# Optimization experiments

Hardware: AMD Instinct MI355X
Metric: run time of the kernel (lower is better)

Reference implementation:

```python
import jax, jax.numpy as jnp
import numpy as np

HIDDEN = 768
HEADS = 12
HEAD_DIM = 64
SEQ = 512
DS_K = 64  # downsampling_k
EPS = 1e-6


def setup_inputs() -> dict:
    key = jax.random.key(0)
    ks = jax.random.split(key, 16)
    B = 32
    sd = 1.0 / DS_K
    glorot = jax.nn.initializers.lecun_normal()  # flax default_kernel_init
    inp = {
        "query": jax.random.normal(ks[0], (B, SEQ, HIDDEN), jnp.float32),
        "key": jax.random.normal(ks[1], (B, SEQ, HIDDEN), jnp.float32),
        "value": jax.random.normal(ks[2], (B, SEQ, HIDDEN), jnp.float32),
        "step": 0,
        # learned Linformer-style downsampling projections [k, s]
        "W_kds": sd * jax.random.normal(ks[3], (DS_K, SEQ), jnp.float32),
        "W_vds": sd * jax.random.normal(ks[4], (DS_K, SEQ), jnp.float32),
        # DenseGeneral qkv kernels [d, n, h] and biases [n, h]
        "Wq": glorot(ks[5], (HIDDEN, HEADS, HEAD_DIM), jnp.float32),
        "bq": jnp.zeros((HEADS, HEAD_DIM), jnp.float32),
        "Wk": glorot(ks[6], (HIDDEN, HEADS, HEAD_DIM), jnp.float32),
        "bk": jnp.zeros((HEADS, HEAD_DIM), jnp.float32),
        "Wv": glorot(ks[7], (HIDDEN, HEADS, HEAD_DIM), jnp.float32),
        "bv": jnp.zeros((HEADS, HEAD_DIM), jnp.float32),
        # out projection contracts (n, h) -> hidden
        "Wout": glorot(ks[8], (HEADS * HEAD_DIM, HIDDEN), jnp.float32).reshape(HEADS, HEAD_DIM, HIDDEN),
        "bout": jnp.zeros((HIDDEN,), jnp.float32),
    }
    return inp


def reference(query, key, value, step, W_kds, W_vds, Wq, bq, Wk, bk, Wv, bv, Wout, bout):
    # Linformer-style downsample of keys/values along sequence: [b,s,d] -> [b,k,d]
    key_ds = jnp.einsum("ks,bsd->bkd", W_kds, key)
    val_ds = jnp.einsum("ks,bsd->bkd", W_vds, value)

    # per-head projections
    queries = jnp.einsum("bqd,dnh->bqnh", query, Wq) + bq    # [b,q,n,h]
    keys = jnp.einsum("bkd,dnh->bknh", key_ds, Wk) + bk      # [b,k,n,h]
    values = jnp.einsum("bkd,dnh->bknh", val_ds, Wv) + bv    # [b,k,n,h]

    # kernelized linear attention with elu feature map (mask=False path)
    phi_q = jax.nn.elu(queries) + 1.0
    phi_k = jax.nn.elu(keys) + 1.0
    s = jnp.einsum("bknd,bknh->bndh", phi_k, values)          # [b,n,h,h] KV state
    z = jnp.sum(phi_k, axis=1)                                 # [b,n,h]
    qs = jnp.einsum("bqnd,bndh->bqnh", phi_q, s)
    qz = jnp.einsum("bqnd,bnd->bqn", phi_q, z) + EPS
    a_v = qs / qz[..., None]                                   # [b,q,n,h]

    out = jnp.einsum("bqnh,nhD->bqD", a_v, Wout) + bout        # [b,q,hidden]
    return out
```

## Files before the change

kernel.cpp:

```cpp
#include <hip/hip_runtime.h>

typedef unsigned short u16;
typedef u16 u16x8 __attribute__((ext_vector_type(8)));
typedef __bf16 bf16;
typedef bf16 bf16x8 __attribute__((ext_vector_type(8)));
typedef float f32x4 __attribute__((ext_vector_type(4)));

__device__ __forceinline__ float bf2f(u16 v) {
  union { unsigned u; float f; } x; x.u = ((unsigned)v) << 16; return x.f;
}
__device__ __forceinline__ u16 f2bf(float f) {
  union { float f; unsigned u; } x; x.f = f;
  unsigned u = x.u;
  u += 0x7fffu + ((u >> 16) & 1u);
  return (u16)(u >> 16);
}

#define GLDS16(g, l) __builtin_amdgcn_global_load_lds( \
    (const __attribute__((address_space(1))) unsigned int*)(const void*)(g), \
    (__attribute__((address_space(3))) unsigned int*)(void*)(l), 16, 0, 0)

__global__ __launch_bounds__(256) void prep_k(
    const float* __restrict__ Wq, const float* __restrict__ Wk,
    const float* __restrict__ Wv, const float* __restrict__ Wout,
    const float* __restrict__ query,
    const float* __restrict__ wkds, const float* __restrict__ wvds,
    const float* __restrict__ b0, const float* __restrict__ b1,
    const float* __restrict__ b2, const float* __restrict__ b3,
    u16* __restrict__ WT, u16* __restrict__ q_bf,
    u16* __restrict__ dstW, u16* __restrict__ dstB)
{
  __shared__ u16 T[64][72];
  const int blk = blockIdx.x;
  const int t = threadIdx.x;
  if (blk < 576) {
    const int bz = blk / 144, rr = blk % 144;
    const int r0 = (rr / 12) * 64, c0 = (rr % 12) * 64;
    const float* W = (bz == 0) ? Wq : (bz == 1) ? Wk : (bz == 2) ? Wv : Wout;
    u16* O = WT + (size_t)bz * 768 * 768;
    #pragma unroll
    for (int p = 0; p < 2; ++p) {
      int v = t + p * 256;
      int r = v / 8, c = (v % 8) * 8;
      f32x4 x0 = *(const f32x4*)&W[(size_t)(r0 + r) * 768 + c0 + c];
      f32x4 x1 = *(const f32x4*)&W[(size_t)(r0 + r) * 768 + c0 + c + 4];
      #pragma unroll
      for (int i = 0; i < 4; ++i) { T[r][c + i] = f2bf(x0[i]); T[r][c + 4 + i] = f2bf(x1[i]); }
    }
    __syncthreads();
    #pragma unroll
    for (int p = 0; p < 2; ++p) {
      int v = t + p * 256;
      int r = v / 8, c = (v % 8) * 8;
      u16x8 tv;
      #pragma unroll
      for (int i = 0; i < 8; ++i) tv[i] = T[c + i][r];
      *(u16x8*)&O[(size_t)(c0 + r) * 768 + r0 + c] = tv;
    }
  } else if (blk < 6720) {
    const size_t i = (size_t)(blk - 576) * 256 + t;
    f32x4 a = *(const f32x4*)&query[i * 8];
    f32x4 b = *(const f32x4*)&query[i * 8 + 4];
    u16x8 w;
    #pragma unroll
    for (int j = 0; j < 4; ++j) { w[j] = f2bf(a[j]); w[4 + j] = f2bf(b[j]); }
    *(u16x8*)&q_bf[i * 8] = w;
  } else {
    const int i = (blk - 6720) * 256 + t;
    if (i < 32768)      dstW[i] = f2bf(wkds[i]);
    else if (i < 65536) dstW[i] = f2bf(wvds[i - 32768]);
    else {
      int j = i - 65536, s = j / 768, si = j % 768;
      const float* src = (s == 0) ? b0 : (s == 1) ? b1 : (s == 2) ? b2 : b3;
      dstB[j] = f2bf(src[si]);
    }
  }
}

__global__ __launch_bounds__(256) void ds_k(
    const u16* __restrict__ Wds,
    const float* __restrict__ key, const float* __restrict__ value,
    u16* __restrict__ key_ds)
{
  __shared__ u16 As[64][40];
  __shared__ u16 Bs[128][36];
  const int pair = blockIdx.y >> 5, b = blockIdx.y & 31;
  const float* src = (pair ? value : key) + (size_t)b * 512 * 768;
  const u16* W = Wds + pair * 32768;
  u16* dst = key_ds + (size_t)pair * 1572864 + (size_t)b * 49152;
  const int nt = blockIdx.x * 128;
  const int t = threadIdx.x, wave = t >> 6, lane = t & 63;
  const int wm = (wave >> 1) * 32, wn = (wave & 1) * 64;
  const int lrow = lane & 15, quad = lane >> 4;
  const int kk = t >> 5, n4 = (t & 31) * 4;

  f32x4 acc[2][4] = {};
  for (int k0 = 0; k0 < 512; k0 += 32) {
    __syncthreads();
    {
      int r = t >> 2, c = (t & 3) * 8;
      *(u16x8*)&As[r][c] = *(const u16x8*)&W[(size_t)r * 512 + k0 + c];
    }
    #pragma unroll
    for (int p = 0; p < 4; ++p) {
      int k = kk + p * 8;
      f32x4 x = *(const f32x4*)&src[(size_t)(k0 + k) * 768 + nt + n4];
      #pragma unroll
      for (int i = 0; i < 4; ++i) Bs[n4 + i][k] = f2bf(x[i]);
    }
    __syncthreads();
    bf16x8 av[2], bv[4];
    #pragma unroll
    for (int i = 0; i < 2; ++i) av[i] = *(const bf16x8*)&As[wm + i * 16 + lrow][quad * 8];
    #pragma unroll
    for (int j = 0; j < 4; ++j) bv[j] = *(const bf16x8*)&Bs[wn + j * 16 + lrow][quad * 8];
    #pragma unroll
    for (int i = 0; i < 2; ++i)
      #pragma unroll
      for (int j = 0; j < 4; ++j)
        acc[i][j] = __builtin_amdgcn_mfma_f32_16x16x32_bf16(av[i], bv[j], acc[i][j], 0, 0, 0);
  }
  #pragma unroll
  for (int i = 0; i < 2; ++i)
    #pragma unroll
    for (int j = 0; j < 4; ++j) {
      const int col = nt + wn + j * 16 + lrow;
      #pragma unroll
      for (int r = 0; r < 4; ++r) {
        const int row = wm + i * 16 + quad * 4 + r;
        dst[(size_t)row * 768 + col] = f2bf(acc[i][j][r]);
      }
    }
}

template<int ACT, bool OF32>
__global__ __launch_bounds__(256) void gemm97_k(
    const u16* __restrict__ A, int lda,
    const u16* __restrict__ Bt, int ldb,
    void* __restrict__ Craw, int ldc,
    const u16* __restrict__ bias, int K)
{
  __shared__ u16 As[128 * 32];
  __shared__ u16 Bs[128 * 32];
  const int mt = blockIdx.x * 128, nt = blockIdx.y * 128;
  const int t = threadIdx.x, wave = t >> 6, lane = t & 63;
  const int wm = (wave >> 1) * 64, wn = (wave & 1) * 64;
  const int lrow = lane & 15, quad = lane >> 4;
  f32x4 acc[4][4] = {};

  for (int k0 = 0; k0 < K; k0 += 32) {
    __syncthreads();
    #pragma unroll
    for (int p = 0; p < 2; ++p) {
      const int s = wave * 128 + p * 64 + lane;
      const int r = s >> 2, c = (s & 3) * 8;
      const int lb = (wave * 128 + p * 64) * 8;
      GLDS16(&A[(size_t)(mt + r) * lda + k0 + c], &As[lb]);
      GLDS16(&Bt[(size_t)(nt + r) * ldb + k0 + c], &Bs[lb]);
    }
    __syncthreads();

    bf16x8 av[4], bv[4];
    #pragma unroll
    for (int i = 0; i < 4; ++i) av[i] = *(const bf16x8*)&As[(wm + i * 16 + lrow) * 32 + quad * 8];
    #pragma unroll
    for (int j = 0; j < 4; ++j) bv[j] = *(const bf16x8*)&Bs[(wn + j * 16 + lrow) * 32 + quad * 8];
    #pragma unroll
    for (int i = 0; i < 4; ++i)
      #pragma unroll
      for (int j = 0; j < 4; ++j)
        acc[i][j] = __builtin_amdgcn_mfma_f32_16x16x32_bf16(av[i], bv[j], acc[i][j], 0, 0, 0);
  }

  #pragma unroll
  for (int i = 0; i < 4; ++i) {
    #pragma unroll
    for (int j = 0; j < 4; ++j) {
      const int col = nt + wn + j * 16 + lrow;
      const float badd = bias ? bf2f(bias[col]) : 0.0f;
      #pragma unroll
      for (int r = 0; r < 4; ++r) {
        const int row = mt + wm + i * 16 + quad * 4 + r;
        float v = acc[i][j][r] + badd;
        if constexpr (ACT == 1) v = v > 0.0f ? v + 1.0f : __expf(v);
        if constexpr (OF32) ((float*)Craw)[(size_t)row * ldc + col] = v;
        else                ((u16*)Craw)[(size_t)row * ldc + col] = f2bf(v);
      }
    }
  }
}

template<int BM, int BN, int BK, int WM, int WN>
__global__ __launch_bounds__(256) void gemmkv_k(
    const u16* __restrict__ A, int lda,
    const u16* __restrict__ B, int ldb,
    u16* __restrict__ C, int ldc,
    const u16* __restrict__ bias,
    int K,
    long long offA_b, long long offB_b, long long offC_b, long long offBias_b)
{
  constexpr int LDSK = BK + 8;
  __shared__ u16 As[BM][LDSK];
  __shared__ u16 Bs[BN][LDSK];
  const int bb = blockIdx.z;
  A += bb * offA_b; B += bb * offB_b; C += bb * offC_b; bias += bb * offBias_b;
  const int mt = blockIdx.x * BM;
  const int nt = blockIdx.y * BN;
  const int t = threadIdx.x;
  const int wave = t >> 6, lane = t & 63;
  constexpr int WAVES_N = BN / WN;
  const int wm = (wave / WAVES_N) * WM;
  const int wn = (wave % WAVES_N) * WN;
  constexpr int FM = WM / 16, FN = WN / 16;
  const int lrow = lane & 15, quad = lane >> 4;
  f32x4 acc[FM][FN] = {};

  for (int k0 = 0; k0 < K; k0 += BK) {
    __syncthreads();
    #pragma unroll
    for (int p = 0; p < (BM * BK / 8) / 256; ++p) {
      int v = t + p * 256;
      int r = v / (BK / 8), c = (v % (BK / 8)) * 8;
      *(u16x8*)&As[r][c] = *(const u16x8*)&A[(size_t)(mt + r) * lda + k0 + c];
    }
    #pragma unroll
    for (int p = 0; p < (BN * BK / 8) / 256; ++p) {
      int v = t + p * 256;
      int r = v / (BK / 8), c = (v % (BK / 8)) * 8;
      *(u16x8*)&Bs[r][c] = *(const u16x8*)&B[(size_t)(nt + r) * ldb + k0 + c];
    }
    __syncthreads();
    bf16x8 av[FM], bv[FN];
    #pragma unroll
    for (int i = 0; i < FM; ++i) av[i] = *(const bf16x8*)&As[wm + i * 16 + lrow][quad * 8];
    #pragma unroll
    for (int j = 0; j < FN; ++j) bv[j] = *(const bf16x8*)&Bs[wn + j * 16 + lrow][quad * 8];
    #pragma unroll
    for (int i = 0; i < FM; ++i)
      #pragma unroll
      for (int j = 0; j < FN; ++j)
        acc[i][j] = __builtin_amdgcn_mfma_f32_16x16x32_bf16(av[i], bv[j], acc[i][j], 0, 0, 0);
  }
  #pragma unroll
  for (int i = 0; i < FM; ++i)
    #pragma unroll
    for (int j = 0; j < FN; ++j) {
      const int col = nt + wn + j * 16 + lrow;
      const float badd = bf2f(bias[col]);
      #pragma unroll
      for (int r = 0; r < 4; ++r) {
        const int row = mt + wm + i * 16 + quad * 4 + r;
        float v = acc[i][j][r] + badd;
        if (bb == 0) v = v > 0.0f ? v + 1.0f : __expf(v);
        C[(size_t)row * ldc + col] = f2bf(v);
      }
    }
}

__global__ __launch_bounds__(256) void kv_state_k(
    const u16* __restrict__ phi_k, const u16* __restrict__ vals,
    u16* __restrict__ sT, float* __restrict__ z)
{
  __shared__ float pk[64][65];
  __shared__ float vv[64][65];
  const int x = blockIdx.x;
  const int b = x / 12, n = x % 12;
  const int t = threadIdx.x;
  const u16* pkg = phi_k + (size_t)b * 64 * 768 + n * 64;
  const u16* vvg = vals  + (size_t)b * 64 * 768 + n * 64;
  #pragma unroll
  for (int p = 0; p < 2; ++p) {
    int v = t + p * 256;
    int r = v / 8, c = (v % 8) * 8;
    u16x8 a  = *(const u16x8*)&pkg[(size_t)r * 768 + c];
    u16x8 bq = *(const u16x8*)&vvg[(size_t)r * 768 + c];
    #pragma unroll
    for (int i = 0; i < 8; ++i) { pk[r][c + i] = bf2f(a[i]); vv[r][c + i] = bf2f(bq[i]); }
  }
  __syncthreads();
  const int d0 = (t >> 4) * 4, h0 = (t & 15) * 4;
  float s4[4][4] = {};
  for (int k = 0; k < 64; ++k) {
    float pv[4], vb[4];
    #pragma unroll
    for (int i = 0; i < 4; ++i) { pv[i] = pk[k][d0 + i]; vb[i] = vv[k][h0 + i]; }
    #pragma unroll
    for (int i = 0; i < 4; ++i)
      #pragma unroll
      for (int j = 0; j < 4; ++j) s4[i][j] += pv[i] * vb[j];
  }
  const size_t base = (size_t)x * 4096;
  #pragma unroll
  for (int i = 0; i < 4; ++i)
    #pragma unroll
    for (int j = 0; j < 4; ++j)
      sT[base + (size_t)(h0 + j) * 64 + d0 + i] = f2bf(s4[i][j]);
  if (t < 64) {
    float zz = 0.f;
    for (int k = 0; k < 64; ++k) zz += pk[k][t];
    z[(size_t)x * 64 + t] = zz;
  }
}

__global__ __launch_bounds__(256) void attn_av_k(
    u16* __restrict__ phi_q, const u16* __restrict__ sT, const float* __restrict__ zbuf)
{
  __shared__ u16 As[64 * 72];
  __shared__ u16 Bs[64 * 72];
  __shared__ float zv[64];
  __shared__ float zpart[4][64];
  __shared__ float zq[64];
  const int x = blockIdx.x, y = blockIdx.y;
  const int b = y / 12, n = y % 12;
  const int t = threadIdx.x;
  u16* Abase = phi_q + (size_t)b * 512 * 768 + (size_t)x * 64 * 768 + n * 64;
  const u16* Bbase = sT + (size_t)y * 4096;
  if (t < 64) zv[t] = zbuf[(size_t)y * 64 + t];
  #pragma unroll
  for (int p = 0; p < 2; ++p) {
    int v = t + p * 256;
    int r = v >> 3, c = (v & 7) * 8;
    *(u16x8*)&As[r * 72 + c] = *(const u16x8*)&Abase[(size_t)r * 768 + c];
    *(u16x8*)&Bs[r * 72 + c] = *(const u16x8*)&Bbase[r * 64 + c];
  }
  __syncthreads();
  {
    int r = t & 63, seg = t >> 6;
    float s = 0.f;
    #pragma unroll
    for (int j = 0; j < 16; ++j) s += bf2f(As[r * 72 + seg * 16 + j]) * zv[seg * 16 + j];
    zpart[seg][r] = s;
  }
  __syncthreads();
  if (t < 64) {
    float s = zpart[0][t] + zpart[1][t] + zpart[2][t] + zpart[3][t];
    zq[t] = 1.0f / (s + 1e-6f);
  }
  const int wave = t >> 6, lane = t & 63;
  const int wm = (wave >> 1) * 32, wn = (wave & 1) * 32;
  const int lrow = lane & 15, quad = lane >> 4;
  f32x4 acc[2][2] = {};
  #pragma unroll
  for (int c = 0; c < 2; ++c) {
    bf16x8 av[2], bv[2];
    #pragma unroll
    for (int i = 0; i < 2; ++i) av[i] = *(const bf16x8*)&As[(wm + i * 16 + lrow) * 72 + c * 32 + quad * 8];
    #pragma unroll
    for (int j = 0; j < 2; ++j) bv[j] = *(const bf16x8*)&Bs[(wn + j * 16 + lrow) * 72 + c * 32 + quad * 8];
    #pragma unroll
    for (int i = 0; i < 2; ++i)
      #pragma unroll
      for (int j = 0; j < 2; ++j)
        acc[i][j] = __builtin_amdgcn_mfma_f32_16x16x32_bf16(av[i], bv[j], acc[i][j], 0, 0, 0);
  }
  __syncthreads();
  #pragma unroll
  for (int i = 0; i < 2; ++i)
    #pragma unroll
    for (int j = 0; j < 2; ++j) {
      const int col = wn + j * 16 + lrow;
      #pragma unroll
      for (int r = 0; r < 4; ++r) {
        const int row = wm + i * 16 + quad * 4 + r;
        Abase[(size_t)row * 768 + col] = f2bf(acc[i][j][r] * zq[row]);
      }
    }
}

__global__ void tagfill_k(float* out, float val, int n) {
  int i = blockIdx.x * 256 + threadIdx.x;
  if (i < n) out[i] = val;
}

extern "C" void kernel_launch(void* const* d_in, const int* in_sizes, int n_in,
                              void* d_out, int out_size, void* d_ws, size_t ws_size,
                              hipStream_t stream) {
  (void)out_size;
  float* out = (float*)d_out;

  int o;
  if (n_in >= 14 && in_sizes[3] == 1) o = 4;
  else if (n_in == 13) o = 3;
  else { tagfill_k<<<4, 256, 0, stream>>>(out, 77.0f, 1024); return; }
  if (in_sizes[0] != 12582912 || in_sizes[o + 0] != 32768 || in_sizes[o + 2] != 589824) {
    tagfill_k<<<4, 256, 0, stream>>>(out, 88.0f, 1024); return;
  }

  const float* query = (const float*)d_in[0];
  const float* key   = (const float*)d_in[1];
  const float* value = (const float*)d_in[2];
  const float* W_kds = (const float*)d_in[o + 0];
  const float* W_vds = (const float*)d_in[o + 1];
  const float* Wq   = (const float*)d_in[o + 2];
  const float* bq   = (const float*)d_in[o + 3];
  const float* Wk   = (const float*)d_in[o + 4];
  const float* bk   = (const float*)d_in[o + 5];
  const float* Wv   = (const float*)d_in[o + 6];
  const float* bv   = (const float*)d_in[o + 7];
  const float* Wout = (const float*)d_in[o + 8];
  const float* bout = (const float*)d_in[o + 9];

  const size_t NEED = 55187456;
  if (ws_size < NEED) { tagfill_k<<<4, 256, 0, stream>>>(out, 123.0f, 1024); return; }

  char* base = (char*)d_ws;
  u16*   WT     = (u16*)base;
  char*  Breg   = base + 4718592;
  u16*   q_bf   = (u16*)Breg;
  u16*   key_ds = (u16*)Breg;
  u16*   sT     = (u16*)Breg;
  float* zbuf   = (float*)(Breg + 3145728);
  u16*   phi_k  = (u16*)(Breg + 6291456);
  u16*   vals   = (u16*)(Breg + 9437184);
  u16*   phi_q  = (u16*)(base + 29884416);
  u16*   Wds_c  = (u16*)(base + 55050240);
  u16*   bias_c = (u16*)(base + 55181312);
  u16* a_v = phi_q;
  u16* WqT   = WT;
  u16* WkT   = WT + 768 * 768;
  u16* WoutT = WT + 3 * 768 * 768;
  u16* bq_c = bias_c, *bk_c = bias_c + 768, *bout_c = bias_c + 2304;

  prep_k<<<6988, 256, 0, stream>>>(Wq, Wk, Wv, Wout, query, W_kds, W_vds,
                                   bq, bk, bv, bout, WT, q_bf, Wds_c, bias_c);

  gemm97_k<1, false><<<dim3(128, 6), 256, 0, stream>>>(
      q_bf, 768, WqT, 768, phi_q, 768, bq_c, 768);

  ds_k<<<dim3(6, 64), 256, 0, stream>>>(Wds_c, key, value, key_ds);

  gemmkv_k<64, 64, 32, 32, 32><<<dim3(32, 12, 2), 256, 0, stream>>>(
      key_ds, 768, WkT, 768, phi_k, 768, bk_c, 768,
      1572864, 589824, 1572864, 768);

  kv_state_k<<<dim3(384), 256, 0, stream>>>(phi_k, vals, sT, zbuf);

  attn_av_k<<<dim3(8, 384), 256, 0, stream>>>(phi_q, sT, zbuf);

  gemm97_k<0, true><<<dim3(128, 6), 256, 0, stream>>>(
      a_v, 768, WoutT, 768, out, 768, bout_c, 768);
}
```

Measured before the change: 312.6 us.

## Pipeline Linformer downsample kernel with register prefetch and double-buffered LDS

The downsample GEMM kernel is restructured. Its N tile shrinks from 128 to 64 columns, doubling the grid to 768 blocks. The A operand (W_ds) now goes straight from global memory into registers, and the fp32 key/value tile is prefetched into registers one K-step ahead. A double-buffered LDS tile allows one barrier per iteration instead of two. The aim is to hide global-load latency and raise occupancy on this memory-bound pass over the key and value tensors, at the cost of per-column scalar strided loads instead of float4 loads.

```diff
diff --git a/kernel.cpp b/kernel.cpp
--- a/kernel.cpp
+++ b/kernel.cpp
@@ -82,48 +82,59 @@
     const float* __restrict__ key, const float* __restrict__ value,
     u16* __restrict__ key_ds)
 {
-  __shared__ u16 As[64][40];
-  __shared__ u16 Bs[128][36];
+  __shared__ u16 Bs[2][64 * 40];
   const int pair = blockIdx.y >> 5, b = blockIdx.y & 31;
   const float* src = (pair ? value : key) + (size_t)b * 512 * 768;
   const u16* W = Wds + pair * 32768;
   u16* dst = key_ds + (size_t)pair * 1572864 + (size_t)b * 49152;
-  const int nt = blockIdx.x * 128;
+  const int nt = blockIdx.x * 64;
   const int t = threadIdx.x, wave = t >> 6, lane = t & 63;
-  const int wm = (wave >> 1) * 32, wn = (wave & 1) * 64;
+  const int wm = (wave >> 1) * 32, wn = (wave & 1) * 32;
   const int lrow = lane & 15, quad = lane >> 4;
-  const int kk = t >> 5, n4 = (t & 31) * 4;
-
-  f32x4 acc[2][4] = {};
-  for (int k0 = 0; k0 < 512; k0 += 32) {
-    __syncthreads();
-    {
-      int r = t >> 2, c = (t & 3) * 8;
-      *(u16x8*)&As[r][c] = *(const u16x8*)&W[(size_t)r * 512 + k0 + c];
-    }
-    #pragma unroll
-    for (int p = 0; p < 4; ++p) {
-      int k = kk + p * 8;
-      f32x4 x = *(const f32x4*)&src[(size_t)(k0 + k) * 768 + nt + n4];
-      #pragma unroll
-      for (int i = 0; i < 4; ++i) Bs[n4 + i][k] = f2bf(x[i]);
-    }
-    __syncthreads();
-    bf16x8 av[2], bv[4];
-    #pragma unroll
-    for (int i = 0; i < 2; ++i) av[i] = *(const bf16x8*)&As[wm + i * 16 + lrow][quad * 8];
-    #pragma unroll
-    for (int j = 0; j < 4; ++j) bv[j] = *(const bf16x8*)&Bs[wn + j * 16 + lrow][quad * 8];
+  const int bn = t & 63, bk8 = (t >> 6) * 8;
+  const float* bcol = src + nt + bn;
+
+  f32x4 acc[2][2] = {};
+  float breg[8];
+  bf16x8 av[2][2];
+
+  #pragma unroll
+  for (int i = 0; i < 8; ++i) breg[i] = bcol[(size_t)(bk8 + i) * 768];
+  #pragma unroll
+  for (int i = 0; i < 2; ++i)
+    av[0][i] = *(const bf16x8*)&W[(size_t)(wm + i * 16 + lrow) * 512 + quad * 8];
+
+  #pragma unroll
+  for (int step = 0; step < 16; ++step) {
+    const int cur = step & 1, nxt = cur ^ 1;
+    u16x8 wv;
+    #pragma unroll
+    for (int i = 0; i < 8; ++i) wv[i] = f2bf(breg[i]);
+    *(u16x8*)&Bs[cur][bn * 40 + bk8] = wv;
+    if (step < 15) {
+      const int k1 = (step + 1) * 32;
+      #pragma unroll
+      for (int i = 0; i < 8; ++i) breg[i] = bcol[(size_t)(k1 + bk8 + i) * 768];
+      #pragma unroll
+      for (int i = 0; i < 2; ++i)
+        av[nxt][i] = *(const bf16x8*)&W[(size_t)(wm + i * 16 + lrow) * 512 + k1 + quad * 8];
+    }
+    __syncthreads();
+    bf16x8 bv[2];
+    #pragma unroll
+    for (int j = 0; j < 2; ++j)
+      bv[j] = *(const bf16x8*)&Bs[cur][(wn + j * 16 + lrow) * 40 + quad * 8];
     #pragma unroll
     for (int i = 0; i < 2; ++i)
       #pragma unroll
-      for (int j = 0; j < 4; ++j)
-        acc[i][j] = __builtin_amdgcn_mfma_f32_16x16x32_bf16(av[i], bv[j], acc[i][j], 0, 0, 0);
-  }
+      for (int j = 0; j < 2; ++j)
+        acc[i][j] = __builtin_amdgcn_mfma_f32_16x16x32_bf16(av[cur][i], bv[j], acc[i][j], 0, 0, 0);
+  }
+
   #pragma unroll
   for (int i = 0; i < 2; ++i)
     #pragma unroll
-    for (int j = 0; j < 4; ++j) {
+    for (int j = 0; j < 2; ++j) {
       const int col = nt + wn + j * 16 + lrow;
       #pragma unroll
       for (int r = 0; r < 4; ++r) {
@@ -427,7 +438,7 @@
   gemm97_k<1, false><<<dim3(128, 6), 256, 0, stream>>>(
       q_bf, 768, WqT, 768, phi_q, 768, bq_c, 768);
 
-  ds_k<<<dim3(6, 64), 256, 0, stream>>>(Wds_c, key, value, key_ds);
+  ds_k<<<dim3(12, 64), 256, 0, stream>>>(Wds_c, key, value, key_ds);
 
   gemmkv_k<64, 64, 32, 32, 32><<<dim3(32, 12, 2), 256, 0, stream>>>(
       key_ds, 768, WkT, 768, phi_k, 768, bk_c, 768,
```

Result: no change. 313.2 us (+0.2%).
